# Optimization experiments

Hardware: AMD Instinct MI355X
Metric: run time of the kernel (lower is better)

The kernel has to match this reference:

```python
import jax, jax.numpy as jnp
import numpy as np

B = 32768      # number of graphs in the batch
NPG = 54       # nodes per graph (fixed by reshape(batch_size, 54*4))
EPG = 144      # directed edges per graph (Catan board: 72 undirected)
N = B * NPG
E = B * EPG
GLOB = 10


def _lin(k, fan_in, fan_out):
    lim = 1.0 / np.sqrt(fan_in)
    kw, kb = jax.random.split(k)
    W = jax.random.uniform(kw, (fan_in, fan_out), jnp.float32, -lim, lim)
    b = jax.random.uniform(kb, (fan_out,), jnp.float32, -lim, lim)
    return W, b


def setup_inputs() -> dict:
    key = jax.random.key(0)
    ks = jax.random.split(key, 16)
    x = jax.random.normal(ks[0], (N, 8), jnp.float32)
    # PyG-style batched edge_index: edges stay within each 54-node block
    base = (jnp.arange(B, dtype=jnp.int32) * NPG)[:, None]
    src = (jax.random.randint(ks[1], (B, EPG), 0, NPG, jnp.int32) + base).reshape(-1)
    dst = (jax.random.randint(ks[2], (B, EPG), 0, NPG, jnp.int32) + base).reshape(-1)
    edge_index = jnp.stack([src, dst], axis=0)
    edge_attr = jax.random.uniform(ks[3], (E,), jnp.float32)
    globalFeats = jax.random.normal(ks[4], (B, GLOB), jnp.float32)
    # GraphConv 1: in=8 -> hidden=16  (lin_rel has bias, lin_root has no bias)
    W_rel1, b1 = _lin(ks[5], 8, 16)
    W_root1, _ = _lin(ks[6], 8, 16)
    # GraphConv 2: 16 -> 4
    W_rel2, b2 = _lin(ks[7], 16, 4)
    W_root2, _ = _lin(ks[8], 16, 4)
    # Global MLP: 10 -> 8 -> 8 -> 10
    Wg1, bg1 = _lin(ks[9], GLOB, 8)
    Wg2, bg2 = _lin(ks[10], 8, 8)
    Wg3, bg3 = _lin(ks[11], 8, GLOB)
    # Out MLP: 54*4 + 10 = 226 -> 128 -> 1
    Wo1, bo1 = _lin(ks[12], NPG * 4 + GLOB, 128)
    Wo2, bo2 = _lin(ks[13], 128, 1)
    return dict(x=x, edge_index=edge_index, edge_attr=edge_attr,
                globalFeats=globalFeats,
                W_rel1=W_rel1, b1=b1, W_root1=W_root1,
                W_rel2=W_rel2, b2=b2, W_root2=W_root2,
                Wg1=Wg1, bg1=bg1, Wg2=Wg2, bg2=bg2, Wg3=Wg3, bg3=bg3,
                Wo1=Wo1, bo1=bo1, Wo2=Wo2, bo2=bo2, isTrain=0)


def _graph_conv(x, src, dst, edge_attr, W_rel, b, W_root):
    # PyG GraphConv (aggr='add'): out = lin_rel(sum_j w_ij * x_j) + lin_root(x)
    msg = edge_attr[:, None] * x[src]                       # [E, F_in]
    agg = jax.ops.segment_sum(msg, dst, num_segments=N)     # [N, F_in]
    return agg @ W_rel + b + x @ W_root


def reference(x, edge_index, edge_attr, globalFeats,
              W_rel1, b1, W_root1, W_rel2, b2, W_root2,
              Wg1, bg1, Wg2, bg2, Wg3, bg3, Wo1, bo1, Wo2, bo2, isTrain):
    src, dst = edge_index[0], edge_index[1]
    h = jax.nn.relu(_graph_conv(x, src, dst, edge_attr, W_rel1, b1, W_root1))
    h = jax.nn.relu(_graph_conv(h, src, dst, edge_attr, W_rel2, b2, W_root2))
    embeds = h.reshape(B, NPG * 4)                          # [B, 216]
    g = jax.nn.relu(globalFeats @ Wg1 + bg1)
    g = jax.nn.relu(g @ Wg2 + bg2)
    g = jax.nn.relu(g @ Wg3 + bg3)
    out = jnp.concatenate([embeds, g], axis=-1)             # [B, 226]
    # dropout p=0.2 with isTrain=0 (eval) -> identity
    out = jax.nn.relu(out @ Wo1 + bo1)
    out = jax.nn.sigmoid(out @ Wo2 + bo2)                   # [B, 1]
    return out
```

## Files before the change

### kernel.cpp

```cpp
#include <hip/hip_runtime.h>
#include <hip/hip_fp16.h>
#include <math.h>

#define NPG 54
#define EPG 144
#define GLOB 10
#define VROW 216
#define GPB 2

typedef _Float16 f16x8 __attribute__((ext_vector_type(8)));
typedef _Float16 f16x4 __attribute__((ext_vector_type(4)));
typedef float    f32x4 __attribute__((ext_vector_type(4)));

#define CFENCE() asm volatile("" ::: "memory")

struct __align__(16) GL {
    _Float16 Adj[NPG][56];
    _Float16 H1T[16][88];
};

__global__ __launch_bounds__(128, 5) void graph_kernel(
    const float* __restrict__ x,
    const int*   __restrict__ edge_index,
    const float* __restrict__ edge_attr,
    const float* __restrict__ W_rel1, const float* __restrict__ b1,
    const float* __restrict__ W_root1,
    const float* __restrict__ W_rel2, const float* __restrict__ b2,
    const float* __restrict__ W_root2,
    _Float16* __restrict__ v_out,
    int E_total)
{
    __shared__ GL S[GPB];
    const int tid  = threadIdx.x;
    const int w    = tid >> 6;
    const int lane = tid & 63;
    const int ln15 = lane & 15;
    const int quad = lane >> 4;
    const int g    = blockIdx.x * GPB + w;
    GL& L = S[w];
    const int nbase = g * NPG;
    const int ebase = g * EPG;

    _Float16* adjp = &L.Adj[0][0];
    _Float16 (*cat)[40] = (_Float16(*)[40])adjp;

    int   esrc_r[3], edst_r[3];
    float ea_r[3];
    #pragma unroll
    for (int k = 0; k < 3; k++) {
        int e = lane + 64 * k;
        if (e < EPG) {
            esrc_r[k] = edge_index[ebase + e] - nbase;
            edst_r[k] = edge_index[(size_t)E_total + ebase + e] - nbase;
            ea_r[k]   = edge_attr[ebase + e];
        } else { esrc_r[k] = 0; edst_r[k] = -1; ea_r[k] = 0.0f; }
    }
    f16x8 xv = {0, 0, 0, 0, 0, 0, 0, 0};
    if (lane < NPG) {
        const float4* xg4 = (const float4*)(x + (size_t)(nbase + lane) * 8);
        float4 lo = xg4[0], hi = xg4[1];
        xv = (f16x8){ (_Float16)lo.x, (_Float16)lo.y, (_Float16)lo.z, (_Float16)lo.w,
                      (_Float16)hi.x, (_Float16)hi.y, (_Float16)hi.z, (_Float16)hi.w };
    }

    f16x8 wf1 = {0, 0, 0, 0, 0, 0, 0, 0};
    if (quad == 0) {
        #pragma unroll
        for (int j = 0; j < 8; j++) wf1[j] = (_Float16)W_rel1[j * 16 + ln15];
    } else if (quad == 1) {
        #pragma unroll
        for (int j = 0; j < 8; j++) wf1[j] = (_Float16)W_root1[j * 16 + ln15];
    }
    f16x8 wf2 = {0, 0, 0, 0, 0, 0, 0, 0};
    if (ln15 < 4) {
        #pragma unroll
        for (int j = 0; j < 8; j++) {
            int k = quad * 8 + j;
            wf2[j] = (_Float16)((k < 16) ? W_rel2[k * 4 + ln15]
                                         : W_root2[(k - 16) * 4 + ln15]);
        }
    }
    const float4 b1q = *(const float4*)(b1 + quad * 4);
    const float4 b2q = *(const float4*)b2;

    {
        uint4* z = (uint4*)&L;
        #pragma unroll
        for (int i = lane; i < 378; i += 64) z[i] = make_uint4(0, 0, 0, 0);
    }
    CFENCE();

    #pragma unroll
    for (int f = 0; f < 8; f++) L.H1T[f][lane] = xv[f];
    {
        uint4* z2 = (uint4*)&L.H1T[8][0];
        #pragma unroll
        for (int i = lane; i < 88; i += 64) z2[i] = make_uint4(0, 0, 0, 0);
    }
    #pragma unroll
    for (int k = 0; k < 3; k++) {
        if (edst_r[k] >= 0) {
            int s = esrc_r[k];
            __half2* cell = (__half2*)&L.Adj[edst_r[k]][s & ~1];
            __half a16 = __float2half(ea_r[k]);
            __half z16 = __float2half(0.0f);
            __half2 val = (s & 1) ? __halves2half2(z16, a16)
                                  : __halves2half2(a16, z16);
            unsafeAtomicAdd(cell, val);
        }
    }
    CFENCE();

    f16x8 af[4][2];
    #pragma unroll
    for (int t = 0; t < 4; t++)
        #pragma unroll
        for (int c = 0; c < 2; c++)
            af[t][c] = *(const f16x8*)(adjp + (t * 16 + ln15) * 56 + c * 32 + quad * 8);
    f16x8 xA[2];
    #pragma unroll
    for (int c = 0; c < 2; c++)
        xA[c] = *(const f16x8*)&L.H1T[ln15][c * 32 + quad * 8];
    CFENCE();

    f32x4 acc1[4];
    #pragma unroll
    for (int t = 0; t < 4; t++) acc1[t] = (f32x4){0.f, 0.f, 0.f, 0.f};
    #pragma unroll
    for (int c = 0; c < 2; c++)
        #pragma unroll
        for (int t = 0; t < 4; t++)
            acc1[t] = __builtin_amdgcn_mfma_f32_16x16x32_f16(xA[c], af[t][c], acc1[t], 0, 0, 0);
    if (quad < 2) {
        #pragma unroll
        for (int t = 0; t < 4; t++) {
            f16x4 ap;
            #pragma unroll
            for (int r = 0; r < 4; r++) ap[r] = (_Float16)acc1[t][r];
            *(f16x4*)&cat[t * 16 + ln15][quad * 4] = ap;
        }
    }
    if (lane < NPG) *(f16x8*)&cat[lane][8] = xv;
    CFENCE();

    f32x4 ci1 = {b1q.x, b1q.y, b1q.z, b1q.w};
    #pragma unroll
    for (int t = 0; t < 4; t++) {
        f16x8 bc = *(const f16x8*)&cat[t * 16 + ln15][quad * 8];
        f32x4 hL = __builtin_amdgcn_mfma_f32_16x16x32_f16(wf1, bc, ci1, 0, 0, 0);
        int node = t * 16 + ln15;
        f16x4 hp;
        #pragma unroll
        for (int r = 0; r < 4; r++) hp[r] = (_Float16)fmaxf(hL[r], 0.0f);
        *(f16x4*)&cat[node][16 + quad * 4] = hp;
        if (node < NPG) {
            #pragma unroll
            for (int r = 0; r < 4; r++) L.H1T[quad * 4 + r][node] = hp[r];
        }
    }
    CFENCE();

    f16x8 hA[2];
    #pragma unroll
    for (int c = 0; c < 2; c++)
        hA[c] = *(const f16x8*)&L.H1T[ln15][c * 32 + quad * 8];
    f32x4 acc2[4];
    #pragma unroll
    for (int t = 0; t < 4; t++) acc2[t] = (f32x4){0.f, 0.f, 0.f, 0.f};
    #pragma unroll
    for (int c = 0; c < 2; c++)
        #pragma unroll
        for (int t = 0; t < 4; t++)
            acc2[t] = __builtin_amdgcn_mfma_f32_16x16x32_f16(hA[c], af[t][c], acc2[t], 0, 0, 0);
    #pragma unroll
    for (int t = 0; t < 4; t++) {
        f16x4 ap;
        #pragma unroll
        for (int r = 0; r < 4; r++) ap[r] = (_Float16)acc2[t][r];
        *(f16x4*)&cat[t * 16 + ln15][quad * 4] = ap;
    }
    CFENCE();

    f32x4 ci2 = {b2q.x, b2q.y, b2q.z, b2q.w};
    #pragma unroll
    for (int t = 0; t < 4; t++) {
        int node = t * 16 + ln15;
        f16x8 bv = *(const f16x8*)&cat[node][quad * 8];
        f32x4 o = __builtin_amdgcn_mfma_f32_16x16x32_f16(wf2, bv, ci2, 0, 0, 0);
        if (quad == 0 && node < NPG) {
            f16x4 vp;
            #pragma unroll
            for (int r = 0; r < 4; r++) vp[r] = (_Float16)fmaxf(o[r], 0.0f);
            *(f16x4*)(v_out + (size_t)g * VROW + node * 4) = vp;
        }
    }
}

#define BTS 264

__global__ __launch_bounds__(320) void wo1t_prep(
    const float* __restrict__ Wo1,
    _Float16* __restrict__ WT)
{
    const int n = blockIdx.x;
    const int k = threadIdx.x;
    if (k < BTS) {
        _Float16 v = (_Float16)0.0f;
        if (k < 226) v = (_Float16)Wo1[(size_t)k * 128 + n];
        WT[(size_t)n * BTS + k] = v;
    }
}

__global__ __launch_bounds__(512) void out_mlp_mfma2(
    const _Float16* __restrict__ V,
    const _Float16* __restrict__ WT,
    const float* __restrict__ gf,
    const float* __restrict__ Wg1, const float* __restrict__ bg1,
    const float* __restrict__ Wg2, const float* __restrict__ bg2,
    const float* __restrict__ Wg3, const float* __restrict__ bg3,
    const float* __restrict__ bo1,
    const float* __restrict__ Wo2,
    const float* __restrict__ bo2,
    float* __restrict__ out)
{
    extern __shared__ _Float16 Bt[];

    const int tid  = threadIdx.x;
    const int w    = tid >> 6;
    const int lane = tid & 63;
    const int ln15 = lane & 15;
    const int quad = lane >> 4;
    const int row0 = blockIdx.x * 128;
    const int row  = row0 + w * 16 + ln15;

    float bo1v[8], wo2v[8];
    #pragma unroll
    for (int t = 0; t < 8; t++) {
        bo1v[t] = bo1[t * 16 + ln15];
        wo2v[t] = Wo2[t * 16 + ln15];
    }
    const float bo2v = bo2[0];

    float t3[GLOB];
    {
        const float* gr = gf + (size_t)row * GLOB;
        float t0[GLOB];
        #pragma unroll
        for (int i = 0; i < GLOB; i++) t0[i] = gr[i];
        float t1[8];
        #pragma unroll
        for (int j = 0; j < 8; j++) {
            float a = bg1[j];
            #pragma unroll
            for (int i = 0; i < GLOB; i++) a += t0[i] * Wg1[i * 8 + j];
            t1[j] = fmaxf(a, 0.0f);
        }
        float t2[8];
        #pragma unroll
        for (int j = 0; j < 8; j++) {
            float a = bg2[j];
            #pragma unroll
            for (int i = 0; i < 8; i++) a += t1[i] * Wg2[i * 8 + j];
            t2[j] = fmaxf(a, 0.0f);
        }
        #pragma unroll
        for (int j = 0; j < GLOB; j++) {
            float a = bg3[j];
            #pragma unroll
            for (int i = 0; i < 8; i++) a += t2[i] * Wg3[i * GLOB + j];
            t3[j] = fmaxf(a, 0.0f);
        }
    }

    const _Float16* Arow = V + (size_t)row * VROW;
    f16x8 af[8];
    #pragma unroll
    for (int s = 0; s < 6; s++)
        af[s] = *(const f16x8*)(Arow + s * 32 + quad * 8);
    if (quad == 3)
        af[6] = (f16x8){ (_Float16)t3[0], (_Float16)t3[1], (_Float16)t3[2], (_Float16)t3[3],
                         (_Float16)t3[4], (_Float16)t3[5], (_Float16)t3[6], (_Float16)t3[7] };
    else
        af[6] = *(const f16x8*)(Arow + 192 + quad * 8);
    af[7] = (f16x8){0, 0, 0, 0, 0, 0, 0, 0};
    if (quad == 0) { af[7][0] = (_Float16)t3[8]; af[7][1] = (_Float16)t3[9]; }

    {
        const int4* wt4 = (const int4*)WT;
        int4* bt4 = (int4*)Bt;
        for (int i = tid; i < 4224; i += 512) bt4[i] = wt4[i];
    }
    __syncthreads();

    f32x4 acc[8];
    #pragma unroll
    for (int t = 0; t < 8; t++) acc[t] = (f32x4){0.f, 0.f, 0.f, 0.f};

    for (int s = 0; s < 8; s++) {
        #pragma unroll
        for (int t = 0; t < 8; t++) {
            f16x8 bf = *(const f16x8*)&Bt[(t * 16 + ln15) * BTS + s * 32 + quad * 8];
            acc[t] = __builtin_amdgcn_mfma_f32_16x16x32_f16(af[s], bf, acc[t], 0, 0, 0);
        }
    }

    #pragma unroll
    for (int rr = 0; rr < 4; rr++) {
        float p = 0.0f;
        #pragma unroll
        for (int t = 0; t < 8; t++) {
            float h = fmaxf(acc[t][rr] + bo1v[t], 0.0f);
            p += h * wo2v[t];
        }
        p += __shfl_xor(p, 1);
        p += __shfl_xor(p, 2);
        p += __shfl_xor(p, 4);
        p += __shfl_xor(p, 8);
        if (ln15 == rr) {
            int orow = row0 + w * 16 + quad * 4 + rr;
            out[orow] = 1.0f / (1.0f + expf(-(p + bo2v)));
        }
    }
}

__global__ __launch_bounds__(512) void out_mlp_mfma(
    const _Float16* __restrict__ V,
    const float* __restrict__ gf,
    const float* __restrict__ Wg1, const float* __restrict__ bg1,
    const float* __restrict__ Wg2, const float* __restrict__ bg2,
    const float* __restrict__ Wg3, const float* __restrict__ bg3,
    const float* __restrict__ Wo1,
    const float* __restrict__ bo1,
    const float* __restrict__ Wo2,
    const float* __restrict__ bo2,
    float* __restrict__ out)
{
    extern __shared__ _Float16 Bt[];

    const int tid  = threadIdx.x;
    const int w    = tid >> 6;
    const int lane = tid & 63;
    const int ln15 = lane & 15;
    const int quad = lane >> 4;
    const int row0 = blockIdx.x * 128;
    const int row  = row0 + w * 16 + ln15;

    float bo1v[8], wo2v[8];
    #pragma unroll
    for (int t = 0; t < 8; t++) {
        bo1v[t] = bo1[t * 16 + ln15];
        wo2v[t] = Wo2[t * 16 + ln15];
    }
    const float bo2v = bo2[0];

    float t3[GLOB];
    {
        const float* gr = gf + (size_t)row * GLOB;
        float t0[GLOB];
        #pragma unroll
        for (int i = 0; i < GLOB; i++) t0[i] = gr[i];
        float t1[8];
        #pragma unroll
        for (int j = 0; j < 8; j++) {
            float a = bg1[j];
            #pragma unroll
            for (int i = 0; i < GLOB; i++) a += t0[i] * Wg1[i * 8 + j];
            t1[j] = fmaxf(a, 0.0f);
        }
        float t2[8];
        #pragma unroll
        for (int j = 0; j < 8; j++) {
            float a = bg2[j];
            #pragma unroll
            for (int i = 0; i < 8; i++) a += t1[i] * Wg2[i * 8 + j];
            t2[j] = fmaxf(a, 0.0f);
        }
        #pragma unroll
        for (int j = 0; j < GLOB; j++) {
            float a = bg3[j];
            #pragma unroll
            for (int i = 0; i < 8; i++) a += t2[i] * Wg3[i * GLOB + j];
            t3[j] = fmaxf(a, 0.0f);
        }
    }

    const _Float16* Arow = V + (size_t)row * VROW;
    f16x8 af[8];
    #pragma unroll
    for (int s = 0; s < 6; s++)
        af[s] = *(const f16x8*)(Arow + s * 32 + quad * 8);
    if (quad == 3)
        af[6] = (f16x8){ (_Float16)t3[0], (_Float16)t3[1], (_Float16)t3[2], (_Float16)t3[3],
                         (_Float16)t3[4], (_Float16)t3[5], (_Float16)t3[6], (_Float16)t3[7] };
    else
        af[6] = *(const f16x8*)(Arow + 192 + quad * 8);
    af[7] = (f16x8){0, 0, 0, 0, 0, 0, 0, 0};
    if (quad == 0) { af[7][0] = (_Float16)t3[8]; af[7][1] = (_Float16)t3[9]; }

    {
        int4* bz = (int4*)Bt;
        for (int i = tid; i < 4224; i += 512)
            bz[i] = make_int4(0, 0, 0, 0);
    }
    __syncthreads();
    for (int i = tid; i < 7232; i += 512) {
        int k  = i >> 5;
        int nq = (i & 31) * 4;
        float4 v = *(const float4*)(Wo1 + (size_t)k * 128 + nq);
        Bt[(nq + 0) * BTS + k] = (_Float16)v.x;
        Bt[(nq + 1) * BTS + k] = (_Float16)v.y;
        Bt[(nq + 2) * BTS + k] = (_Float16)v.z;
        Bt[(nq + 3) * BTS + k] = (_Float16)v.w;
    }
    __syncthreads();

    f32x4 acc[8];
    #pragma unroll
    for (int t = 0; t < 8; t++) acc[t] = (f32x4){0.f, 0.f, 0.f, 0.f};

    for (int s = 0; s < 8; s++) {
        #pragma unroll
        for (int t = 0; t < 8; t++) {
            f16x8 bf = *(const f16x8*)&Bt[(t * 16 + ln15) * BTS + s * 32 + quad * 8];
            acc[t] = __builtin_amdgcn_mfma_f32_16x16x32_f16(af[s], bf, acc[t], 0, 0, 0);
        }
    }

    #pragma unroll
    for (int rr = 0; rr < 4; rr++) {
        float p = 0.0f;
        #pragma unroll
        for (int t = 0; t < 8; t++) {
            float h = fmaxf(acc[t][rr] + bo1v[t], 0.0f);
            p += h * wo2v[t];
        }
        p += __shfl_xor(p, 1);
        p += __shfl_xor(p, 2);
        p += __shfl_xor(p, 4);
        p += __shfl_xor(p, 8);
        if (ln15 == rr) {
            int orow = row0 + w * 16 + quad * 4 + rr;
            out[orow] = 1.0f / (1.0f + expf(-(p + bo2v)));
        }
    }
}

extern "C" void kernel_launch(void* const* d_in, const int* in_sizes, int n_in,
                              void* d_out, int out_size, void* d_ws, size_t ws_size,
                              hipStream_t stream) {
    const float* x        = (const float*)d_in[0];
    const int*   ei       = (const int*)  d_in[1];
    const float* ea       = (const float*)d_in[2];
    const float* gf       = (const float*)d_in[3];
    const float* W_rel1   = (const float*)d_in[4];
    const float* b1       = (const float*)d_in[5];
    const float* W_root1  = (const float*)d_in[6];
    const float* W_rel2   = (const float*)d_in[7];
    const float* b2       = (const float*)d_in[8];
    const float* W_root2  = (const float*)d_in[9];
    const float* Wg1      = (const float*)d_in[10];
    const float* bg1      = (const float*)d_in[11];
    const float* Wg2      = (const float*)d_in[12];
    const float* bg2      = (const float*)d_in[13];
    const float* Wg3      = (const float*)d_in[14];
    const float* bg3      = (const float*)d_in[15];
    const float* Wo1      = (const float*)d_in[16];
    const float* bo1      = (const float*)d_in[17];
    const float* Wo2      = (const float*)d_in[18];
    const float* bo2      = (const float*)d_in[19];

    float* out   = (float*)d_out;
    _Float16* V  = (_Float16*)d_ws;

    const int B = out_size;
    const int E = in_sizes[1] / 2;

    const size_t VBYTES  = (size_t)B * VROW * sizeof(_Float16);
    const size_t WTBYTES = (size_t)128 * BTS * sizeof(_Float16);
    _Float16* WT = (_Float16*)((char*)d_ws + VBYTES);
    const bool use_prep = (ws_size >= VBYTES + WTBYTES);

    if (use_prep)
        wo1t_prep<<<128, 320, 0, stream>>>(Wo1, WT);

    graph_kernel<<<B / GPB, 128, 0, stream>>>(
        x, ei, ea,
        W_rel1, b1, W_root1, W_rel2, b2, W_root2,
        V, E);

    if (use_prep)
        out_mlp_mfma2<<<B / 128, 512, 128 * BTS * sizeof(_Float16), stream>>>(
            V, WT, gf, Wg1, bg1, Wg2, bg2, Wg3, bg3, bo1, Wo2, bo2, out);
    else
        out_mlp_mfma<<<B / 128, 512, 128 * BTS * sizeof(_Float16), stream>>>(
            V, gf, Wg1, bg1, Wg2, bg2, Wg3, bg3, Wo1, bo1, Wo2, bo2, out);
}
```

Baseline: 203.2 us.

## Split each graph across two wavefronts instead of one wave per graph

Each block now processes a single graph with two wavefronts. Each wave owns half of the 16-row node tiles and half of the edge and feature loads, with __syncthreads between stages. This cuts the per-wave serial work and register use (launch bounds raised to 8) and doubles the grid size. In exchange it adds block barriers and halves LDS per block, which may change occupancy behaviour.

```diff
diff --git a/kernel.cpp b/kernel.cpp
--- a/kernel.cpp
+++ b/kernel.cpp
@@ -6,7 +6,6 @@
 #define EPG 144
 #define GLOB 10
 #define VROW 216
-#define GPB 2
 
 typedef _Float16 f16x8 __attribute__((ext_vector_type(8)));
 typedef _Float16 f16x4 __attribute__((ext_vector_type(4)));
@@ -19,7 +18,7 @@
     _Float16 H1T[16][88];
 };
 
-__global__ __launch_bounds__(128, 5) void graph_kernel(
+__global__ __launch_bounds__(128, 8) void graph_kernel(
     const float* __restrict__ x,
     const int*   __restrict__ edge_index,
     const float* __restrict__ edge_attr,
@@ -30,34 +29,35 @@
     _Float16* __restrict__ v_out,
     int E_total)
 {
-    __shared__ GL S[GPB];
+    __shared__ GL L;
     const int tid  = threadIdx.x;
     const int w    = tid >> 6;
     const int lane = tid & 63;
     const int ln15 = lane & 15;
     const int quad = lane >> 4;
-    const int g    = blockIdx.x * GPB + w;
-    GL& L = S[w];
+    const int g    = blockIdx.x;
     const int nbase = g * NPG;
     const int ebase = g * EPG;
+    const int t0   = 2 * w;
 
     _Float16* adjp = &L.Adj[0][0];
     _Float16 (*cat)[40] = (_Float16(*)[40])adjp;
 
-    int   esrc_r[3], edst_r[3];
-    float ea_r[3];
-    #pragma unroll
-    for (int k = 0; k < 3; k++) {
-        int e = lane + 64 * k;
-        if (e < EPG) {
-            esrc_r[k] = edge_index[ebase + e] - nbase;
-            edst_r[k] = edge_index[(size_t)E_total + ebase + e] - nbase;
-            ea_r[k]   = edge_attr[ebase + e];
-        } else { esrc_r[k] = 0; edst_r[k] = -1; ea_r[k] = 0.0f; }
-    }
+    const int e0 = (w == 0) ? lane : 64 + lane;
+    int   es0 = edge_index[ebase + e0] - nbase;
+    int   ed0 = edge_index[(size_t)E_total + ebase + e0] - nbase;
+    float ea0 = edge_attr[ebase + e0];
+    int es1 = 0, ed1 = -1; float ea1 = 0.0f;
+    if (w == 0 && lane < 16) {
+        const int e1 = 128 + lane;
+        es1 = edge_index[ebase + e1] - nbase;
+        ed1 = edge_index[(size_t)E_total + ebase + e1] - nbase;
+        ea1 = edge_attr[ebase + e1];
+    }
+    const int xrow = w * 32 + lane;
     f16x8 xv = {0, 0, 0, 0, 0, 0, 0, 0};
-    if (lane < NPG) {
-        const float4* xg4 = (const float4*)(x + (size_t)(nbase + lane) * 8);
+    if (lane < 32 && xrow < NPG) {
+        const float4* xg4 = (const float4*)(x + (size_t)(nbase + xrow) * 8);
         float4 lo = xg4[0], hi = xg4[1];
         xv = (f16x8){ (_Float16)lo.x, (_Float16)lo.y, (_Float16)lo.z, (_Float16)lo.w,
                       (_Float16)hi.x, (_Float16)hi.y, (_Float16)hi.z, (_Float16)hi.w };
@@ -86,69 +86,71 @@
     {
         uint4* z = (uint4*)&L;
         #pragma unroll
-        for (int i = lane; i < 378; i += 64) z[i] = make_uint4(0, 0, 0, 0);
-    }
-    CFENCE();
-
-    #pragma unroll
-    for (int f = 0; f < 8; f++) L.H1T[f][lane] = xv[f];
-    {
+        for (int i = tid; i < 378; i += 128) z[i] = make_uint4(0, 0, 0, 0);
         uint4* z2 = (uint4*)&L.H1T[8][0];
-        #pragma unroll
-        for (int i = lane; i < 88; i += 64) z2[i] = make_uint4(0, 0, 0, 0);
-    }
-    #pragma unroll
-    for (int k = 0; k < 3; k++) {
-        if (edst_r[k] >= 0) {
-            int s = esrc_r[k];
-            __half2* cell = (__half2*)&L.Adj[edst_r[k]][s & ~1];
-            __half a16 = __float2half(ea_r[k]);
-            __half z16 = __float2half(0.0f);
-            __half2 val = (s & 1) ? __halves2half2(z16, a16)
-                                  : __halves2half2(a16, z16);
-            unsafeAtomicAdd(cell, val);
-        }
-    }
-    CFENCE();
-
-    f16x8 af[4][2];
-    #pragma unroll
-    for (int t = 0; t < 4; t++)
+        if (tid < 88) z2[tid] = make_uint4(0, 0, 0, 0);
+    }
+    if (lane < 32) {
+        #pragma unroll
+        for (int f = 0; f < 8; f++) L.H1T[f][xrow] = xv[f];
+    }
+    __syncthreads();
+
+    {
+        __half2* cell = (__half2*)&L.Adj[ed0][es0 & ~1];
+        __half a16 = __float2half(ea0);
+        __half z16 = __float2half(0.0f);
+        __half2 val = (es0 & 1) ? __halves2half2(z16, a16)
+                                : __halves2half2(a16, z16);
+        unsafeAtomicAdd(cell, val);
+    }
+    if (ed1 >= 0) {
+        __half2* cell = (__half2*)&L.Adj[ed1][es1 & ~1];
+        __half a16 = __float2half(ea1);
+        __half z16 = __float2half(0.0f);
+        __half2 val = (es1 & 1) ? __halves2half2(z16, a16)
+                                : __halves2half2(a16, z16);
+        unsafeAtomicAdd(cell, val);
+    }
+    __syncthreads();
+
+    f16x8 af[2][2];
+    #pragma unroll
+    for (int tt = 0; tt < 2; tt++)
         #pragma unroll
         for (int c = 0; c < 2; c++)
-            af[t][c] = *(const f16x8*)(adjp + (t * 16 + ln15) * 56 + c * 32 + quad * 8);
+            af[tt][c] = *(const f16x8*)(adjp + ((t0 + tt) * 16 + ln15) * 56 + c * 32 + quad * 8);
     f16x8 xA[2];
     #pragma unroll
     for (int c = 0; c < 2; c++)
         xA[c] = *(const f16x8*)&L.H1T[ln15][c * 32 + quad * 8];
+    f32x4 acc1[2];
+    #pragma unroll
+    for (int tt = 0; tt < 2; tt++) acc1[tt] = (f32x4){0.f, 0.f, 0.f, 0.f};
+    #pragma unroll
+    for (int c = 0; c < 2; c++)
+        #pragma unroll
+        for (int tt = 0; tt < 2; tt++)
+            acc1[tt] = __builtin_amdgcn_mfma_f32_16x16x32_f16(xA[c], af[tt][c], acc1[tt], 0, 0, 0);
+    __syncthreads();
+
+    if (quad < 2) {
+        #pragma unroll
+        for (int tt = 0; tt < 2; tt++) {
+            f16x4 ap;
+            #pragma unroll
+            for (int r = 0; r < 4; r++) ap[r] = (_Float16)acc1[tt][r];
+            *(f16x4*)&cat[(t0 + tt) * 16 + ln15][quad * 4] = ap;
+        }
+    }
+    if (lane < 32 && xrow < NPG) *(f16x8*)&cat[xrow][8] = xv;
     CFENCE();
-
-    f32x4 acc1[4];
-    #pragma unroll
-    for (int t = 0; t < 4; t++) acc1[t] = (f32x4){0.f, 0.f, 0.f, 0.f};
-    #pragma unroll
-    for (int c = 0; c < 2; c++)
-        #pragma unroll
-        for (int t = 0; t < 4; t++)
-            acc1[t] = __builtin_amdgcn_mfma_f32_16x16x32_f16(xA[c], af[t][c], acc1[t], 0, 0, 0);
-    if (quad < 2) {
-        #pragma unroll
-        for (int t = 0; t < 4; t++) {
-            f16x4 ap;
-            #pragma unroll
-            for (int r = 0; r < 4; r++) ap[r] = (_Float16)acc1[t][r];
-            *(f16x4*)&cat[t * 16 + ln15][quad * 4] = ap;
-        }
-    }
-    if (lane < NPG) *(f16x8*)&cat[lane][8] = xv;
-    CFENCE();
-
     f32x4 ci1 = {b1q.x, b1q.y, b1q.z, b1q.w};
     #pragma unroll
-    for (int t = 0; t < 4; t++) {
-        f16x8 bc = *(const f16x8*)&cat[t * 16 + ln15][quad * 8];
+    for (int tt = 0; tt < 2; tt++) {
+        f16x8 bc = *(const f16x8*)&cat[(t0 + tt) * 16 + ln15][quad * 8];
         f32x4 hL = __builtin_amdgcn_mfma_f32_16x16x32_f16(wf1, bc, ci1, 0, 0, 0);
-        int node = t * 16 + ln15;
+        int node = (t0 + tt) * 16 + ln15;
         f16x4 hp;
         #pragma unroll
         for (int r = 0; r < 4; r++) hp[r] = (_Float16)fmaxf(hL[r], 0.0f);
@@ -158,33 +160,32 @@
             for (int r = 0; r < 4; r++) L.H1T[quad * 4 + r][node] = hp[r];
         }
     }
-    CFENCE();
+    __syncthreads();
 
     f16x8 hA[2];
     #pragma unroll
     for (int c = 0; c < 2; c++)
         hA[c] = *(const f16x8*)&L.H1T[ln15][c * 32 + quad * 8];
-    f32x4 acc2[4];
-    #pragma unroll
-    for (int t = 0; t < 4; t++) acc2[t] = (f32x4){0.f, 0.f, 0.f, 0.f};
+    f32x4 acc2[2];
+    #pragma unroll
+    for (int tt = 0; tt < 2; tt++) acc2[tt] = (f32x4){0.f, 0.f, 0.f, 0.f};
     #pragma unroll
     for (int c = 0; c < 2; c++)
         #pragma unroll
-        for (int t = 0; t < 4; t++)
-            acc2[t] = __builtin_amdgcn_mfma_f32_16x16x32_f16(hA[c], af[t][c], acc2[t], 0, 0, 0);
-    #pragma unroll
-    for (int t = 0; t < 4; t++) {
+        for (int tt = 0; tt < 2; tt++)
+            acc2[tt] = __builtin_amdgcn_mfma_f32_16x16x32_f16(hA[c], af[tt][c], acc2[tt], 0, 0, 0);
+    #pragma unroll
+    for (int tt = 0; tt < 2; tt++) {
         f16x4 ap;
         #pragma unroll
-        for (int r = 0; r < 4; r++) ap[r] = (_Float16)acc2[t][r];
-        *(f16x4*)&cat[t * 16 + ln15][quad * 4] = ap;
+        for (int r = 0; r < 4; r++) ap[r] = (_Float16)acc2[tt][r];
+        *(f16x4*)&cat[(t0 + tt) * 16 + ln15][quad * 4] = ap;
     }
     CFENCE();
-
     f32x4 ci2 = {b2q.x, b2q.y, b2q.z, b2q.w};
     #pragma unroll
-    for (int t = 0; t < 4; t++) {
-        int node = t * 16 + ln15;
+    for (int tt = 0; tt < 2; tt++) {
+        int node = (t0 + tt) * 16 + ln15;
         f16x8 bv = *(const f16x8*)&cat[node][quad * 8];
         f32x4 o = __builtin_amdgcn_mfma_f32_16x16x32_f16(wf2, bv, ci2, 0, 0, 0);
         if (quad == 0 && node < NPG) {
@@ -483,7 +484,7 @@
     if (use_prep)
         wo1t_prep<<<128, 320, 0, stream>>>(Wo1, WT);
 
-    graph_kernel<<<B / GPB, 128, 0, stream>>>(
+    graph_kernel<<<B, 128, 0, stream>>>(
         x, ei, ea,
         W_rel1, b1, W_root1, W_rel2, b2, W_root2,
         V, E);
```

After: 206.0 us. Within noise of the previous version (+1.4%).
